# Kernel optimization log

Measured on AMD Instinct MI355X. Metric: run time of the kernel, lower is better.

The kernel has to match this reference:

```python
import jax, jax.numpy as jnp
import numpy as np

N = 20000; P = 3; L_LP = 10; L_NS = 20; D = 128; OUT = 2; E = 640000; V_LP = 5000; V_NS = 10000


def _gru(x, lengths, W_ih, W_hh, b_ih, b_hh):
    # x: [B, T, Din]; returns last valid hidden state per sequence (pack_padded semantics)
    T = x.shape[1]
    xp = jnp.einsum('btd,gd->btg', x, W_ih) + b_ih  # [B, T, 3H]
    h0 = jnp.zeros((x.shape[0], W_hh.shape[1]), x.dtype)

    def step(h, inp):
        xpt, t = inp
        hp = h @ W_hh.T + b_hh
        xr, xz, xn = jnp.split(xpt, 3, axis=-1)
        hr, hz, hn = jnp.split(hp, 3, axis=-1)
        r = jax.nn.sigmoid(xr + hr)
        z = jax.nn.sigmoid(xz + hz)
        nn_ = jnp.tanh(xn + r * hn)
        h_new = (1.0 - z) * nn_ + z * h
        h = jnp.where((t < lengths)[:, None], h_new, h)
        return h, None

    hT, _ = jax.lax.scan(step, h0, (jnp.swapaxes(xp, 0, 1), jnp.arange(T)))
    return hT


def _gcn(x, src, dst, w, W, b, n):
    # PyG GCNConv: add self-loops (weight 1), symmetric normalization by in-degree
    loops = jnp.arange(n)
    s = jnp.concatenate([src, loops])
    d = jnp.concatenate([dst, loops])
    ww = jnp.concatenate([w, jnp.ones((n,), w.dtype)])
    deg = jax.ops.segment_sum(ww, d, num_segments=n)
    dinv = jnp.where(deg > 0, 1.0 / jnp.sqrt(deg), 0.0)
    norm = dinv[s] * ww * dinv[d]
    xw = x @ W.T
    return jax.ops.segment_sum(norm[:, None] * xw[s], d, num_segments=n) + b


def _lnorm(x, g, b):
    m = jnp.mean(x, axis=-1, keepdims=True)
    v = jnp.var(x, axis=-1, keepdims=True)
    return (x - m) / jnp.sqrt(v + 1e-5) * g + b


def _forward(x_ref, x_def, x_pdt, edge_weight, lp_emb, ns_emb, lp_Wih, lp_Whh, lp_bih, lp_bhh, ns_Wih, ns_Whh, ns_bih, ns_bhh, lp_fc_W, lp_fc_b, all_fc_W, all_fc_b, conv1_W, conv1_b, conv2_W, conv2_b, conv3_W, conv3_b, ln1_g, ln1_b, ln2_g, ln2_b, mp1_W, mp1_b, mp2_W, mp2_b, idx_lp, x_lp_length, idx_ns, x_ns_length, edge_index):
    n = idx_ns.shape[0]
    # long-path GRU encodings, one GRU run per path slot (vmapped over P)
    xl = lp_emb[idx_lp]  # [N, P, L_LP, D]
    gru_lp = lambda seq, lens: _gru(seq, lens, lp_Wih, lp_Whh, lp_bih, lp_bhh)
    h_lp = jax.vmap(gru_lp, in_axes=(1, 1))(xl, x_lp_length)  # [P, N, D]
    # torch.cat(h_list).view(N, D*P): row-major reshape of [P, N, D]
    x_lp = h_lp.reshape(n, P * D) @ lp_fc_W.T + lp_fc_b
    # natural-sequence GRU encoding
    x_ns = _gru(ns_emb[idx_ns], x_ns_length, ns_Wih, ns_Whh, ns_bih, ns_bhh)  # [N, D]
    # torch.cat(dim=0).view(N, 5D): faithful row-major reshape of [5N, D]
    x = jnp.concatenate([x_pdt, x_ref, x_def, x_lp, x_ns], axis=0).reshape(n, 5 * D)
    x = x @ all_fc_W.T + all_fc_b
    src, dst = edge_index[0], edge_index[1]
    convs = [(conv1_W, conv1_b), (conv2_W, conv2_b), (conv3_W, conv3_b)]
    lns = [(ln1_g, ln1_b), (ln2_g, ln2_b)]
    emb = x
    for i in range(3):
        x = _gcn(x, src, dst, edge_weight, convs[i][0], convs[i][1], n)
        emb = x
        x = jax.nn.relu(x)
        # dropout p=0.25 omitted (eval mode)
        if i < 2:
            x = _lnorm(x, lns[i][0], lns[i][1])
    x = x @ mp1_W.T + mp1_b
    x = x @ mp2_W.T + mp2_b
    return emb, jax.nn.log_softmax(x, axis=1)


def setup_inputs() -> dict:
    ks = jax.random.split(jax.random.key(0), 40)
    f32 = jnp.float32
    nrm = lambda k, sh, s: jax.random.normal(k, sh, f32) * s
    inp = {}
    inp['idx_lp'] = jax.random.randint(ks[0], (N, P, L_LP), 0, V_LP)
    inp['x_lp_length'] = jax.random.randint(ks[1], (N, P), 1, L_LP + 1)
    inp['idx_ns'] = jax.random.randint(ks[2], (N, L_NS), 0, V_NS)
    inp['x_ns_length'] = jax.random.randint(ks[3], (N,), 1, L_NS + 1)
    inp['x_ref'] = nrm(ks[4], (N, D), 1.0)
    inp['x_def'] = nrm(ks[5], (N, D), 1.0)
    inp['x_pdt'] = nrm(ks[6], (N, D), 1.0)
    inp['edge_index'] = jax.random.randint(ks[7], (2, E), 0, N)
    inp['edge_weight'] = jax.random.uniform(ks[8], (E,), f32)
    inp['lp_emb'] = nrm(ks[9], (V_LP, D), 0.5)
    inp['ns_emb'] = nrm(ks[10], (V_NS, D), 0.5)
    s = 0.08
    inp['lp_Wih'] = nrm(ks[11], (3 * D, D), s)
    inp['lp_Whh'] = nrm(ks[12], (3 * D, D), s)
    inp['lp_bih'] = nrm(ks[13], (3 * D,), s)
    inp['lp_bhh'] = nrm(ks[14], (3 * D,), s)
    inp['ns_Wih'] = nrm(ks[15], (3 * D, D), s)
    inp['ns_Whh'] = nrm(ks[16], (3 * D, D), s)
    inp['ns_bih'] = nrm(ks[17], (3 * D,), s)
    inp['ns_bhh'] = nrm(ks[18], (3 * D,), s)
    inp['lp_fc_W'] = nrm(ks[19], (D, P * D), 0.05)
    inp['lp_fc_b'] = nrm(ks[20], (D,), 0.05)
    inp['all_fc_W'] = nrm(ks[21], (D, 5 * D), 0.05)
    inp['all_fc_b'] = nrm(ks[22], (D,), 0.05)
    inp['conv1_W'] = nrm(ks[23], (D, D), 0.08)
    inp['conv1_b'] = nrm(ks[24], (D,), 0.05)
    inp['conv2_W'] = nrm(ks[25], (D, D), 0.08)
    inp['conv2_b'] = nrm(ks[26], (D,), 0.05)
    inp['conv3_W'] = nrm(ks[27], (D, D), 0.08)
    inp['conv3_b'] = nrm(ks[28], (D,), 0.05)
    inp['ln1_g'] = jnp.ones((D,), f32)
    inp['ln1_b'] = jnp.zeros((D,), f32)
    inp['ln2_g'] = jnp.ones((D,), f32)
    inp['ln2_b'] = jnp.zeros((D,), f32)
    inp['mp1_W'] = nrm(ks[29], (D, D), 0.08)
    inp['mp1_b'] = nrm(ks[30], (D,), 0.05)
    inp['mp2_W'] = nrm(ks[31], (OUT, D), 0.08)
    inp['mp2_b'] = nrm(ks[32], (OUT,), 0.05)
    return inp


def reference(idx_lp, x_lp_length, idx_ns, x_ns_length, x_ref, x_def, x_pdt, edge_index, edge_weight, lp_emb, ns_emb, lp_Wih, lp_Whh, lp_bih, lp_bhh, ns_Wih, ns_Whh, ns_bih, ns_bhh, lp_fc_W, lp_fc_b, all_fc_W, all_fc_b, conv1_W, conv1_b, conv2_W, conv2_b, conv3_W, conv3_b, ln1_g, ln1_b, ln2_g, ln2_b, mp1_W, mp1_b, mp2_W, mp2_b):
    return _forward(x_ref, x_def, x_pdt, edge_weight, lp_emb, ns_emb, lp_Wih, lp_Whh, lp_bih, lp_bhh, ns_Wih, ns_Whh, ns_bih, ns_bhh, lp_fc_W, lp_fc_b, all_fc_W, all_fc_b, conv1_W, conv1_b, conv2_W, conv2_b, conv3_W, conv3_b, ln1_g, ln1_b, ln2_g, ln2_b, mp1_W, mp1_b, mp2_W, mp2_b, idx_lp, x_lp_length, idx_ns, x_ns_length, edge_index)
```

## Files before the change

kernel.cpp:

```cpp
#include <hip/hip_runtime.h>
#include <math.h>

typedef unsigned short u16;
typedef short bf16x4 __attribute__((ext_vector_type(4)));
typedef short bf16x8 __attribute__((ext_vector_type(8)));
typedef float f32x16 __attribute__((ext_vector_type(16)));

#define NN 20000
#define PP 3
#define TLP 10
#define TNS 20
#define DD 128
#define EE 640000

__device__ __forceinline__ float bf2f(u16 u) {
  union { unsigned u; float f; } v; v.u = ((unsigned)u) << 16; return v.f;
}
__device__ __forceinline__ u16 f2bf(float f) {
  union { float f; unsigned u; } v; v.f = f;
  unsigned r = v.u + 0x7fffu + ((v.u >> 16) & 1u);
  return (u16)(r >> 16);
}
__device__ __forceinline__ short f2bf_hw(float f) {
  __bf16 b = (__bf16)f;
  return (short)__builtin_bit_cast(unsigned short, b);
}
__device__ __forceinline__ float loadf(const void* p, size_t i, int isf) {
  return isf ? ((const float*)p)[i] : bf2f(((const u16*)p)[i]);
}
__device__ __forceinline__ float fex2(float x) { return __builtin_amdgcn_exp2f(x); }
__device__ __forceinline__ float frcp(float x) { return __builtin_amdgcn_rcpf(x); }
__device__ __forceinline__ unsigned cvtpk(float lo, float hi) {
  unsigned r; asm("v_cvt_pk_bf16_f32 %0, %1, %2" : "=v"(r) : "v"(lo), "v"(hi));
  return r;
}

__global__ void k_detect(const void* probe, int* flag, int* bins) {
  __shared__ int any;
  if (threadIdx.x == 0) any = 0;
  __syncthreads();
  if (threadIdx.x < 128) bins[threadIdx.x] = 0;
  const u16* p = (const u16*)probe;
  int bad = 0;
  for (int i = threadIdx.x; i < 4096; i += 256) {
    int e = (p[2 * i] >> 7) & 0xFF;
    if (e >= 0x9F) bad = 1;
  }
  if (bad) atomicOr(&any, 1);
  __syncthreads();
  if (threadIdx.x == 0) flag[0] = any;
}

struct CvtJobs {
  const void* src[16];
  int off[16];
  int n[16];
};

struct CvtJobsB {
  const void* src[12];
  int off[12];
  int n[12];
  int thr[12];
  float scA[12];
  float scB[12];
};

__global__ void k_cvtb(CvtJobsB j, CvtJobs jf, u16* __restrict__ dst,
                       float* __restrict__ fdst, int* __restrict__ counts,
                       const int* flag) {
  const int isf = flag[0];
  if (blockIdx.x >= 12 * 64 + 16) {
    int i = (blockIdx.x - (12 * 64 + 16)) * 256 + threadIdx.x;
    if (i < NN) counts[i] = 0;
    return;
  }
  if (blockIdx.x >= 12 * 64) {
    const int job = blockIdx.x - 12 * 64;
    const void* s = jf.src[job];
    float* d = fdst + jf.off[job];
    const int n = jf.n[job];
    for (int i = threadIdx.x; i < n; i += 256) d[i] = loadf(s, i, isf);
    return;
  }
  const int job = blockIdx.x >> 6;
  if (job < 2 && !isf) return;
  const int chunk = blockIdx.x & 63;
  const void* s = j.src[job];
  u16* d = dst + j.off[job];
  const int n = j.n[job];
  const int thr = j.thr[job];
  const float sA = j.scA[job], sB = j.scB[job];
  for (int i = chunk * 256 + threadIdx.x; i < n; i += 64 * 256)
    d[i] = f2bf(loadf(s, i, isf) * (i < thr ? sA : sB));
}

__global__ void k_lenboth(const int* __restrict__ lensLP,
                          const int* __restrict__ lensNS,
                          int* __restrict__ bins) {
  int sg = blockIdx.x * 256 + threadIdx.x;
  int lane = threadIdx.x & 63;
  int binL = 0, binN = 0;
  if (sg < PP * NN) binL = lensLP[(sg % NN) * PP + sg / NN];
  if (sg < NN) binN = lensNS[sg];
  for (int b = 1; b <= TLP; ++b) {
    unsigned long long m = __ballot(binL == b);
    if (m) {
      int leader = (int)(__ffsll((long long)m) - 1);
      if (lane == leader) atomicAdd(&bins[b], (int)__popcll(m));
    }
  }
  for (int b = 1; b <= TNS; ++b) {
    unsigned long long m = __ballot(binN == b);
    if (m) {
      int leader = (int)(__ffsll((long long)m) - 1);
      if (lane == leader) atomicAdd(&bins[64 + b], (int)__popcll(m));
    }
  }
}

__global__ void k_binscan2(int* __restrict__ bins,
                           const float* __restrict__ w_mp2,
                           const float* __restrict__ b_mp1_,
                           const float* __restrict__ b_mp2_,
                           const void* __restrict__ mp1raw,
                           float* __restrict__ Wc, const int* flag) {
  if (blockIdx.x == 0) {
    if (threadIdx.x == 0) {
      int acc = 0;
      for (int k = 0; k < 32; ++k) { bins[32 + k] = acc; acc += bins[k]; }
    }
    if (threadIdx.x == 1) {
      int acc = 0;
      for (int k = 0; k < 32; ++k) { bins[96 + k] = acc; acc += bins[64 + k]; }
    }
    return;
  }
  const int isf = flag[0];
  const int t = threadIdx.x;
  const int o = t >> 7, k = t & 127;
  float acc = 0.f;
  for (int d2 = 0; d2 < 128; ++d2)
    acc += w_mp2[o * 128 + d2] * loadf(mp1raw, (size_t)d2 * 128 + k, isf);
  Wc[t] = acc;
  if (t < 2) {
    float bacc = b_mp2_[t];
    for (int d2 = 0; d2 < 128; ++d2) bacc += w_mp2[t * 128 + d2] * b_mp1_[d2];
    Wc[256 + t] = bacc;
  }
}

__global__ void k_lenfillboth(const int* __restrict__ lensLP,
                              const int* __restrict__ lensNS,
                              int* __restrict__ bins,
                              int* __restrict__ permLP,
                              int* __restrict__ permNS) {
  int sg = blockIdx.x * 256 + threadIdx.x;
  int lane = threadIdx.x & 63;
  int binL = 0, binN = 0;
  if (sg < PP * NN) binL = lensLP[(sg % NN) * PP + sg / NN];
  if (sg < NN) binN = lensNS[sg];
  for (int b = 1; b <= TLP; ++b) {
    unsigned long long m = __ballot(binL == b);
    if (m) {
      int leader = (int)(__ffsll((long long)m) - 1);
      int base = 0;
      if (lane == leader) base = atomicAdd(&bins[32 + b], (int)__popcll(m));
      base = __shfl(base, leader);
      if (binL == b) {
        int rank = (int)__popcll(m & ((1ull << lane) - 1ull));
        permLP[base + rank] = sg;
      }
    }
  }
  for (int b = 1; b <= TNS; ++b) {
    unsigned long long m = __ballot(binN == b);
    if (m) {
      int leader = (int)(__ffsll((long long)m) - 1);
      int base = 0;
      if (lane == leader) base = atomicAdd(&bins[96 + b], (int)__popcll(m));
      base = __shfl(base, leader);
      if (binN == b) {
        int rank = (int)__popcll(m & ((1ull << lane) - 1ull));
        permNS[base + rank] = sg;
      }
    }
  }
}

__global__ __launch_bounds__(512, 2) void k_gru5(
    const int* __restrict__ permLP, const int* __restrict__ permNS, int nbNS,
    const u16* __restrict__ embLPc, const u16* __restrict__ embNSc,
    const u16* __restrict__ embLPr, const u16* __restrict__ embNSr,
    const int* __restrict__ idxLP, const int* __restrict__ idxNS,
    const int* __restrict__ lenLP, const int* __restrict__ lenNS,
    const u16* __restrict__ WihLP, const u16* __restrict__ WhhLP,
    const u16* __restrict__ WihNS, const u16* __restrict__ WhhNS,
    const float* __restrict__ bihLP, const float* __restrict__ bhhLP,
    const float* __restrict__ bihNS, const float* __restrict__ bhhNS,
    u16* __restrict__ HoutLP, u16* __restrict__ HoutNS, int nbLP,
    const int* __restrict__ e_dst, int* __restrict__ counts,
    const int* __restrict__ flag) {
  __shared__ u16 xp[2][3][128][36];
  __shared__ u16 Hbf2[2][32][132];
  __shared__ int ivs[TNS][32];
  __shared__ int rowv[32], outv[32], lenv_s[32];
  __shared__ int Tbs;

  const int bid = blockIdx.x;
  const int nGru = nbLP + nbNS;
  const int tid = threadIdx.x;
  if (bid >= nGru) {
    int e = (bid - nGru) * 512 + tid;
    if (e < EE) atomicAdd(&counts[e_dst[e]], 1);
    return;
  }
  const int isf = flag[0];
  const int isNS = bid < nbNS;
  const int chunk = isNS ? (nbNS - 1 - bid) : (nbLP - 1 - (bid - nbNS));
  const int* perm = isNS ? (permNS + chunk * 32) : (permLP + chunk * 32);
  const u16* embbf = isNS ? (isf ? embNSc : embNSr) : (isf ? embLPc : embLPr);
  const int* idx = isNS ? idxNS : idxLP;
  const int* lens = isNS ? lenNS : lenLP;
  const u16* Wih = isNS ? WihNS : WihLP;
  const u16* Whh = isNS ? WhhNS : WhhLP;
  const float* bih = isNS ? bihNS : bihLP;
  const float* bhh = isNS ? bhhNS : bhhLP;
  u16* Hout = isNS ? HoutNS : HoutLP;
  const int T = isNS ? TNS : TLP;

  const int w = tid >> 6, lane = tid & 63;
  const int l31 = lane & 31, lh = lane >> 5;
  const int role = w >> 2;
  const int j = w & 3;
  const int d = 32 * j + l31;

  if (tid < 32) {
    int sg = perm[tid];
    int row = isNS ? sg : ((sg % NN) * PP + sg / NN);
    rowv[tid] = row;
    outv[tid] = sg;
    lenv_s[tid] = lens[row];
  }
  __syncthreads();
  if (tid == 0) {
    int m = 1;
    for (int k = 0; k < 32; ++k) m = max(m, lenv_s[k]);
    Tbs = m;
  }
  __syncthreads();
  const int Tb = Tbs;

  for (int z = tid; z < Tb * 32; z += 512) {
    int s = z & 31, t = z >> 5;
    ivs[t][s] = idx[(size_t)rowv[s] * T + t];
  }
  for (int z = tid; z < 2112; z += 512) ((unsigned*)Hbf2[0])[z] = 0u;

  bf16x8 wf[24];
  {
    const u16* Ws = role ? Whh : Wih;
#pragma unroll
    for (int g = 0; g < 3; ++g)
#pragma unroll
      for (int kb = 0; kb < 8; ++kb)
        wf[g * 8 + kb] =
            *(const bf16x8*)(Ws + (size_t)(128 * g + d) * 128 + kb * 16 + lh * 8);
  }
  const float SA = -1.44269504088896f;
  const float SN = -2.88539008177793f;
  float ib0, ib1, ib2;
  if (!role) {
    ib0 = SA * (bih[d] + bhh[d]);
    ib1 = SA * (bih[128 + d] + bhh[128 + d]);
    ib2 = SN * bih[256 + d];
  } else {
    ib0 = 0.f;
    ib1 = 0.f;
    ib2 = SN * bhh[256 + d];
  }

  __syncthreads();
  int lenr[16];
#pragma unroll
  for (int rg = 0; rg < 16; ++rg)
    lenr[rg] = lenv_s[(rg & 3) + 8 * (rg >> 2) + 4 * lh];

  float h[16];
#pragma unroll
  for (int rg = 0; rg < 16; ++rg) h[rg] = 0.f;

  for (int i = 0; i <= Tb; ++i) {
    if (!role) {
      if (i < Tb) {
        bf16x8 Xf[8];
        const u16* erow = embbf + (size_t)ivs[i][l31] * 128 + lh * 8;
#pragma unroll
        for (int kb = 0; kb < 8; ++kb) Xf[kb] = *(const bf16x8*)(erow + kb * 16);
        f32x16 a0 = (f32x16)(ib0), a1 = (f32x16)(ib1), a2 = (f32x16)(ib2);
#pragma unroll
        for (int kb = 0; kb < 8; ++kb) {
          a0 = __builtin_amdgcn_mfma_f32_32x32x16_bf16(Xf[kb], wf[kb], a0, 0, 0, 0);
          a1 = __builtin_amdgcn_mfma_f32_32x32x16_bf16(Xf[kb], wf[8 + kb], a1, 0, 0, 0);
          a2 = __builtin_amdgcn_mfma_f32_32x32x16_bf16(Xf[kb], wf[16 + kb], a2, 0, 0, 0);
        }
        const int sl = i & 1;
#pragma unroll
        for (int rq = 0; rq < 4; ++rq) {
          int mo = 8 * rq + 4 * lh;
          bf16x4 p0, p1, p2;
#pragma unroll
          for (int q = 0; q < 4; ++q) {
            p0[q] = f2bf_hw(a0[4 * rq + q]);
            p1[q] = f2bf_hw(a1[4 * rq + q]);
            p2[q] = f2bf_hw(a2[4 * rq + q]);
          }
          *(bf16x4*)(&xp[sl][0][d][mo]) = p0;
          *(bf16x4*)(&xp[sl][1][d][mo]) = p1;
          *(bf16x4*)(&xp[sl][2][d][mo]) = p2;
        }
      }
    } else {
      if (i >= 1) {
        const int rs = (i - 1) & 1, wsl = i & 1;
        bf16x8 Hf[8];
#pragma unroll
        for (int kb = 0; kb < 8; ++kb) {
          bf16x4 lo = *(const bf16x4*)(&Hbf2[rs][l31][16 * kb + 8 * lh]);
          bf16x4 hi = *(const bf16x4*)(&Hbf2[rs][l31][16 * kb + 8 * lh + 4]);
          Hf[kb] = __builtin_shufflevector(lo, hi, 0, 1, 2, 3, 4, 5, 6, 7);
        }
        f32x16 a0 = (f32x16)(ib0), a1 = (f32x16)(ib1), a2 = (f32x16)(ib2);
#pragma unroll
        for (int kb = 0; kb < 8; ++kb) {
          a0 = __builtin_amdgcn_mfma_f32_32x32x16_bf16(Hf[kb], wf[kb], a0, 0, 0, 0);
          a1 = __builtin_amdgcn_mfma_f32_32x32x16_bf16(Hf[kb], wf[8 + kb], a1, 0, 0, 0);
          a2 = __builtin_amdgcn_mfma_f32_32x32x16_bf16(Hf[kb], wf[16 + kb], a2, 0, 0, 0);
        }
        const int t = i - 1;
#pragma unroll
        for (int rq = 0; rq < 4; ++rq) {
          int mo = 8 * rq + 4 * lh;
          bf16x4 x0 = *(const bf16x4*)(&xp[rs][0][d][mo]);
          bf16x4 x1 = *(const bf16x4*)(&xp[rs][1][d][mo]);
          bf16x4 x2 = *(const bf16x4*)(&xp[rs][2][d][mo]);
          float hq[4];
#pragma unroll
          for (int q = 0; q < 4; ++q) {
            int rg = 4 * rq + q;
            float r = frcp(1.f + fex2(a0[rg] + bf2f((u16)x0[q])));
            float z = frcp(1.f + fex2(a1[rg] + bf2f((u16)x1[q])));
            float s = fmaf(r, a2[rg], bf2f((u16)x2[q]));
            float nn_ = fmaf(2.f, frcp(1.f + fex2(s)), -1.f);
            float hnew = fmaf(z, h[rg] - nn_, nn_);
            h[rg] = (t < lenr[rg]) ? hnew : h[rg];
            hq[q] = h[rg];
          }
          unsigned pa = cvtpk(hq[0], hq[1]);
          unsigned pb = cvtpk(hq[2], hq[3]);
          Hbf2[wsl][mo + 0][d] = (u16)pa;
          Hbf2[wsl][mo + 1][d] = (u16)(pa >> 16);
          Hbf2[wsl][mo + 2][d] = (u16)pb;
          Hbf2[wsl][mo + 3][d] = (u16)(pb >> 16);
        }
      }
    }
    __syncthreads();
  }

  if (role) {
#pragma unroll
    for (int rg = 0; rg < 16; ++rg) {
      int m = (rg & 3) + 8 * (rg >> 2) + 4 * lh;
      Hout[(size_t)outv[m] * 128 + d] = f2bf(h[rg]);
    }
  }
}

__global__ __launch_bounds__(128) void k_gemm_mfma(
    const void* __restrict__ A0, const void* __restrict__ A1,
    const void* __restrict__ A2, const u16* __restrict__ A3,
    const u16* __restrict__ A4, int mode, int K,
    const u16* __restrict__ W, const float* __restrict__ bias,
    void* __restrict__ Cout, int out_bf, int M, const int* __restrict__ flag,
    const int* __restrict__ esrc, const int* __restrict__ edst,
    const void* __restrict__ ew, int* __restrict__ cursor,
    int2* __restrict__ csr, const int* __restrict__ startT,
    float* __restrict__ dinvOut, int tailN, int tailMode, int gemmBlocks) {
  const int isf = flag[0];
  const int tid = threadIdx.x;
  if ((int)blockIdx.x >= gemmBlocks) {
    int i = ((int)blockIdx.x - gemmBlocks) * 128 + tid;
    if (i < tailN) {
      if (tailMode == 1) {
        int s = esrc[i];
        float wv = loadf(ew, i, isf);
        int p = atomicAdd(&cursor[edst[i]], 1);
        csr[p] = make_int2(s, __float_as_int(wv));
      } else {
        int a = startT[i], b = startT[i + 1];
        float sum = 1.f;
        for (int k = a; k < b; ++k) sum += __int_as_float(csr[k].y);
        dinvOut[i] = 1.f / sqrtf(sum);
      }
    }
    return;
  }
  const int w = tid >> 6, lane = tid & 63;
  const int l31 = lane & 31, lh = lane >> 5;
  const int w23 = w;
  const int mbase = blockIdx.x * 32;
  const int row = mbase + l31;
  const int rowc = row < M ? row : M - 1;

  f32x16 acc0 = (f32x16)(0.f), acc1 = (f32x16)(0.f);
  const int nk = K >> 4;
  for (int kb = 0; kb < nk; ++kb) {
    bf16x8 a;
    if (mode == 0) {
      a = *(const bf16x8*)((const u16*)A0 + (size_t)rowc * K + kb * 16 + lh * 8);
    } else {
      int r5 = 5 * rowc + (kb >> 3);
      int slot = r5 / NN;
      int inner = r5 - slot * NN;
      int koff = (kb & 7) * 16 + lh * 8;
      if (slot < 3) {
        const void* p = (slot == 0) ? A0 : (slot == 1) ? A1 : A2;
        if (isf) {
          const float* fp = (const float*)p + (size_t)inner * 128 + koff;
          float4 v0 = *(const float4*)fp;
          float4 v1 = *(const float4*)(fp + 4);
          a[0] = (short)f2bf(v0.x); a[1] = (short)f2bf(v0.y);
          a[2] = (short)f2bf(v0.z); a[3] = (short)f2bf(v0.w);
          a[4] = (short)f2bf(v1.x); a[5] = (short)f2bf(v1.y);
          a[6] = (short)f2bf(v1.z); a[7] = (short)f2bf(v1.w);
        } else {
          a = *(const bf16x8*)((const u16*)p + (size_t)inner * 128 + koff);
        }
      } else {
        const u16* p = (slot == 3) ? A3 : A4;
        a = *(const bf16x8*)(p + (size_t)inner * 128 + koff);
      }
    }
    const u16* wp = W + (size_t)(64 * w23 + l31) * K + kb * 16 + lh * 8;
    bf16x8 b0 = *(const bf16x8*)wp;
    bf16x8 b1 = *(const bf16x8*)(wp + (size_t)32 * K);
    acc0 = __builtin_amdgcn_mfma_f32_32x32x16_bf16(a, b0, acc0, 0, 0, 0);
    acc1 = __builtin_amdgcn_mfma_f32_32x32x16_bf16(a, b1, acc1, 0, 0, 0);
  }
  const int col0 = 64 * w23 + l31;
  const float bv0 = bias ? bias[col0] : 0.f;
  const float bv1 = bias ? bias[col0 + 32] : 0.f;
#pragma unroll
  for (int rg = 0; rg < 16; ++rg) {
    int m = (rg & 3) + 8 * (rg >> 2) + 4 * lh;
    int grow = mbase + m;
    if (grow < M) {
      float v0 = acc0[rg] + bv0, v1 = acc1[rg] + bv1;
      if (out_bf) {
        ((u16*)Cout)[(size_t)grow * 128 + col0] = f2bf(v0);
        ((u16*)Cout)[(size_t)grow * 128 + col0 + 32] = f2bf(v1);
      } else {
        ((float*)Cout)[(size_t)grow * 128 + col0] = v0;
        ((float*)Cout)[(size_t)grow * 128 + col0 + 32] = v1;
      }
    }
  }
}

__global__ void k_scan(const int* __restrict__ counts, int* __restrict__ start,
                       int* __restrict__ cursor, int n) {
  __shared__ int part[256];
  const int C = (n + 255) / 256;
  int tid = threadIdx.x;
  int base = tid * C;
  int s = 0;
  for (int k = 0; k < C; ++k) {
    int i = base + k;
    s += (i < n) ? counts[i] : 0;
  }
  part[tid] = s;
  __syncthreads();
  if (tid == 0) {
    int acc = 0;
    for (int k = 0; k < 256; ++k) { int v = part[k]; part[k] = acc; acc += v; }
  }
  __syncthreads();
  int run = part[tid];
  for (int k = 0; k < C; ++k) {
    int i = base + k;
    if (i < n) {
      int c = counts[i];
      start[i] = run;
      cursor[i] = run;
      run += c;
    }
  }
  if (tid == 255) start[n] = run;
}

__global__ __launch_bounds__(256) void k_gcn_gather(
    const int* __restrict__ start, const int2* __restrict__ csr,
    const float* __restrict__ dinv, const u16* __restrict__ xwbf,
    const float* __restrict__ bias, const float* __restrict__ g,
    const float* __restrict__ b, u16* __restrict__ out_bf,
    void* __restrict__ dout, const float* __restrict__ Wc,
    const int* __restrict__ flag, int mode) {
  int v = blockIdx.x * 4 + (threadIdx.x >> 6);
  int lane = threadIdx.x & 63;
  if (v >= NN) return;
  const int c0 = 2 * lane;
  float acc0 = 0.f, acc1 = 0.f;
  int i = start[v];
  const int i1 = start[v + 1];
  for (; i + 4 <= i1; i += 4) {
    int2 e0 = csr[i], e1 = csr[i + 1], e2 = csr[i + 2], e3 = csr[i + 3];
    unsigned p0 = *(const unsigned*)(xwbf + (size_t)e0.x * 128 + c0);
    unsigned p1 = *(const unsigned*)(xwbf + (size_t)e1.x * 128 + c0);
    unsigned p2 = *(const unsigned*)(xwbf + (size_t)e2.x * 128 + c0);
    unsigned p3 = *(const unsigned*)(xwbf + (size_t)e3.x * 128 + c0);
    float f0 = __int_as_float(e0.y) * dinv[e0.x];
    float f1 = __int_as_float(e1.y) * dinv[e1.x];
    float f2 = __int_as_float(e2.y) * dinv[e2.x];
    float f3 = __int_as_float(e3.y) * dinv[e3.x];
    acc0 += f0 * bf2f((u16)(p0 & 0xffff)) + f1 * bf2f((u16)(p1 & 0xffff)) +
            f2 * bf2f((u16)(p2 & 0xffff)) + f3 * bf2f((u16)(p3 & 0xffff));
    acc1 += f0 * bf2f((u16)(p0 >> 16)) + f1 * bf2f((u16)(p1 >> 16)) +
            f2 * bf2f((u16)(p2 >> 16)) + f3 * bf2f((u16)(p3 >> 16));
  }
  if (i + 2 <= i1) {
    int2 e0 = csr[i], e1 = csr[i + 1];
    unsigned p0 = *(const unsigned*)(xwbf + (size_t)e0.x * 128 + c0);
    unsigned p1 = *(const unsigned*)(xwbf + (size_t)e1.x * 128 + c0);
    float f0 = __int_as_float(e0.y) * dinv[e0.x];
    float f1 = __int_as_float(e1.y) * dinv[e1.x];
    acc0 += f0 * bf2f((u16)(p0 & 0xffff)) + f1 * bf2f((u16)(p1 & 0xffff));
    acc1 += f0 * bf2f((u16)(p0 >> 16)) + f1 * bf2f((u16)(p1 >> 16));
    i += 2;
  }
  if (i < i1) {
    int2 e = csr[i];
    float c = __int_as_float(e.y) * dinv[e.x];
    unsigned pv = *(const unsigned*)(xwbf + (size_t)e.x * 128 + c0);
    acc0 += c * bf2f((u16)(pv & 0xffff));
    acc1 += c * bf2f((u16)(pv >> 16));
  }
  float dv = dinv[v];
  unsigned sv = *(const unsigned*)(xwbf + (size_t)v * 128 + c0);
  float y0 = bias[c0] + dv * (dv * bf2f((u16)(sv & 0xffff)) + acc0);
  float y1 = bias[c0 + 1] + dv * (dv * bf2f((u16)(sv >> 16)) + acc1);
  if (mode == 1) {
    if (flag[0]) {
      *(float2*)((float*)dout + (size_t)v * 128 + c0) = make_float2(y0, y1);
    } else {
      unsigned pk = (unsigned)f2bf(y0) | ((unsigned)f2bf(y1) << 16);
      *(unsigned*)((u16*)dout + (size_t)v * 128 + c0) = pk;
    }
    float x0 = fmaxf(y0, 0.f), x1 = fmaxf(y1, 0.f);
    float p0 = x0 * Wc[c0] + x1 * Wc[c0 + 1];
    float p1 = x0 * Wc[128 + c0] + x1 * Wc[128 + c0 + 1];
#pragma unroll
    for (int off = 32; off; off >>= 1) {
      p0 += __shfl_xor(p0, off);
      p1 += __shfl_xor(p1, off);
    }
    if (lane == 0) {
      float v0 = p0 + Wc[256], v1 = p1 + Wc[257];
      float m = fmaxf(v0, v1);
      float ls = m + logf(__expf(v0 - m) + __expf(v1 - m));
      size_t base = (size_t)NN * 128 + (size_t)v * 2;
      if (flag[0]) {
        ((float*)dout)[base + 0] = v0 - ls;
        ((float*)dout)[base + 1] = v1 - ls;
      } else {
        unsigned pk = (unsigned)f2bf(v0 - ls) | ((unsigned)f2bf(v1 - ls) << 16);
        *(unsigned*)((u16*)dout + base) = pk;
      }
    }
  } else {
    float x0 = fmaxf(y0, 0.f), x1 = fmaxf(y1, 0.f);
    float s_ = x0 + x1;
#pragma unroll
    for (int off = 32; off; off >>= 1) s_ += __shfl_xor(s_, off);
    float mean = s_ * (1.f / 128.f);
    float e0 = x0 - mean, e1 = x1 - mean;
    float vv = e0 * e0 + e1 * e1;
#pragma unroll
    for (int off = 32; off; off >>= 1) vv += __shfl_xor(vv, off);
    float inv = 1.f / sqrtf(vv * (1.f / 128.f) + 1e-5f);
    unsigned pk = (unsigned)f2bf(e0 * inv * g[c0] + b[c0]) |
                  ((unsigned)f2bf(e1 * inv * g[c0 + 1] + b[c0 + 1]) << 16);
    *(unsigned*)(out_bf + (size_t)v * 128 + c0) = pk;
  }
}

extern "C" void kernel_launch(void* const* d_in, const int* in_sizes, int n_in,
                              void* d_out, int out_size, void* d_ws, size_t ws_size,
                              hipStream_t stream) {
  const int* idx_lp = (const int*)d_in[0];
  const int* len_lp = (const int*)d_in[1];
  const int* idx_ns = (const int*)d_in[2];
  const int* len_ns = (const int*)d_in[3];
  const void* x_ref = d_in[4];
  const void* x_def = d_in[5];
  const void* x_pdt = d_in[6];
  const int* eidx   = (const int*)d_in[7];
  const void* ew    = d_in[8];
  const void* lp_emb = d_in[9];
  const void* ns_emb = d_in[10];

  char* cur = (char*)d_ws;
  auto alloc = [&](size_t bytes, size_t align) -> void* {
    size_t a = ((size_t)cur + align - 1) & ~(align - 1);
    cur = (char*)(a + bytes);
    return (void*)a;
  };
  int* flag     = (int*)alloc(64, 64);
  float* smallW = (float*)alloc(3104 * 4, 16);
  float* f_Wc   = (float*)alloc(260 * 4, 16);
  float* f_dinv = (float*)alloc(NN * 4, 16);
  int* counts   = (int*)alloc(NN * 4, 16);
  int* startA   = (int*)alloc((NN + 1) * 4, 16);
  int* cursorE  = (int*)alloc(NN * 4, 16);
  int* bins     = (int*)alloc(128 * 4, 16);
  int* perm_lp  = (int*)alloc(PP * NN * 4, 16);
  int* perm_ns  = (int*)alloc(NN * 4, 16);
  int2* csr2    = (int2*)alloc((size_t)EE * 8, 16);
  u16* ub       = (u16*)alloc((size_t)20233216 * 2, 16);
  u16* embbf_lp = ub;
  u16* embbf_ns = ub + 640000;
  u16* wg_lpih  = ub + 1920000;
  u16* wg_lphh  = ub + 1969152;
  u16* wg_nsih  = ub + 2018304;
  u16* wg_nshh  = ub + 2067456;
  u16* wg_lpfc  = ub + 2116608;
  u16* wg_allfc = ub + 2165760;
  u16* wg_c1    = ub + 2247680;
  u16* wg_c2    = ub + 2264064;
  u16* wg_c3    = ub + 2280448;
  u16* hbf_lp   = ub + 2313216;
  u16* hbf_ns   = ub + 9993216;
  u16* lp_bf    = ub + 12553216;
  u16* xcur_bf  = ub + 15113216;
  u16* xw_bf    = ub + 17673216;

  static const int fn[16] = {384, 384, 384, 384, 128, 128, 128, 128,
                             128, 128, 128, 128, 128, 128, 256, 2};
  static const int fsrc[16] = {13, 14, 17, 18, 20, 22, 24, 26,
                               28, 29, 30, 31, 32, 34, 35, 36};
  CvtJobs jf;
  int foff[16];
  {
    int off = 0;
    for (int j = 0; j < 16; ++j) {
      jf.src[j] = d_in[fsrc[j]];
      jf.off[j] = off;
      jf.n[j] = fn[j];
      foff[j] = off;
      off += fn[j];
    }
  }
  float* b_lpbih = smallW + foff[0];
  float* b_lpbhh = smallW + foff[1];
  float* b_nsbih = smallW + foff[2];
  float* b_nsbhh = smallW + foff[3];
  float* b_lpfc  = smallW + foff[4];
  float* b_allfc = smallW + foff[5];
  float* b_conv[3] = {smallW + foff[6], smallW + foff[7], smallW + foff[8]};
  float* g_ln[2] = {smallW + foff[9], smallW + foff[11]};
  float* b_ln[2] = {smallW + foff[10], smallW + foff[12]};
  float* b_mp1   = smallW + foff[13];
  float* w_mp2   = smallW + foff[14];
  float* b_mp2   = smallW + foff[15];

  static const int bn[12] = {640000, 1280000, 49152, 49152, 49152, 49152,
                             49152, 81920, 16384, 16384, 16384, 0};
  static const int bsrc[12] = {9, 10, 11, 12, 15, 16, 19, 21, 23, 25, 27, 33};
  static const int boff[12] = {0, 640000, 1920000, 1969152, 2018304, 2067456,
                               2116608, 2165760, 2247680, 2264064, 2280448,
                               2296832};
  CvtJobsB jb;
  for (int j = 0; j < 12; ++j) {
    jb.src[j] = d_in[bsrc[j]];
    jb.off[j] = boff[j];
    jb.n[j] = bn[j];
    const bool gw = (j >= 2 && j <= 5);
    jb.thr[j] = gw ? 32768 : 0;
    jb.scA[j] = gw ? -1.44269504088896f : 1.f;
    jb.scB[j] = gw ? -2.88539008177793f : 1.f;
  }

  const int* e_src = eidx;
  const int* e_dst = eidx + EE;

  k_detect<<<1, 256, 0, stream>>>(lp_emb, flag, bins);

  const int initBlocks = (NN + 255) / 256;
  k_cvtb<<<12 * 64 + 16 + initBlocks, 256, 0, stream>>>(jb, jf, ub, smallW,
                                                        counts, flag);

  k_lenboth<<<(PP * NN + 255) / 256, 256, 0, stream>>>(len_lp, len_ns, bins);
  k_binscan2<<<2, 256, 0, stream>>>(bins, w_mp2, b_mp1, b_mp2, d_in[33],
                                    f_Wc, flag);
  k_lenfillboth<<<(PP * NN + 255) / 256, 256, 0, stream>>>(len_lp, len_ns, bins,
                                                           perm_lp, perm_ns);

  const int nbLP = PP * NN / 32, nbNS = NN / 32;
  const int histBlocks = (EE + 511) / 512;
  k_gru5<<<nbLP + nbNS + histBlocks, 512, 0, stream>>>(
      perm_lp, perm_ns, nbNS, embbf_lp, embbf_ns,
      (const u16*)lp_emb, (const u16*)ns_emb,
      idx_lp, idx_ns, len_lp, len_ns,
      wg_lpih, wg_lphh, wg_nsih, wg_nshh, b_lpbih, b_lpbhh, b_nsbih, b_nsbhh,
      hbf_lp, hbf_ns, nbLP, e_dst, counts, flag);

  k_scan<<<1, 256, 0, stream>>>(counts, startA, cursorE, NN);

  const int gg = (NN + 31) / 32;
  const int fillBlocks = (EE + 127) / 128;
  const int degBlocks = (NN + 127) / 128;
  k_gemm_mfma<<<gg + fillBlocks, 128, 0, stream>>>(
      hbf_lp, nullptr, nullptr, nullptr, nullptr, 0, 384, wg_lpfc, b_lpfc,
      lp_bf, 1, NN, flag, e_src, e_dst, ew, cursorE, csr2, nullptr, nullptr,
      EE, 1, gg);
  k_gemm_mfma<<<gg + degBlocks, 128, 0, stream>>>(
      x_pdt, x_ref, x_def, lp_bf, hbf_ns, 1, 640, wg_allfc, b_allfc,
      xcur_bf, 1, NN, flag, nullptr, nullptr, nullptr, nullptr, csr2, startA,
      f_dinv, NN, 2, gg);

  const u16* wgc[3] = {wg_c1, wg_c2, wg_c3};
  for (int l = 0; l < 3; ++l) {
    k_gemm_mfma<<<gg, 128, 0, stream>>>(
        xcur_bf, nullptr, nullptr, nullptr, nullptr, 0, DD, wgc[l], nullptr,
        xw_bf, 1, NN, flag, nullptr, nullptr, nullptr, nullptr, nullptr,
        nullptr, nullptr, 0, 0, gg);
    if (l < 2) {
      k_gcn_gather<<<NN / 4, 256, 0, stream>>>(startA, csr2, f_dinv, xw_bf,
                                               b_conv[l], g_ln[l], b_ln[l],
                                               xcur_bf, nullptr, nullptr,
                                               flag, 0);
    } else {
      k_gcn_gather<<<NN / 4, 256, 0, stream>>>(startA, csr2, f_dinv, xw_bf,
                                               b_conv[l], nullptr, nullptr,
                                               nullptr, d_out, f_Wc,
                                               flag, 1);
    }
  }
}
```

Measured before the change: 898.9 us.

## Move edge histogram into length-binning kernel and fold scan into GRU launch

The per-destination edge count histogram now runs as extra blocks of the earlier k_lenboth kernel instead of as tail blocks of the GRU kernel. The exclusive scan over counts, which produces the CSR start and cursor arrays, becomes block 0 of the GRU kernel, so the separate single-block k_scan launch goes away. This cuts one kernel launch and hides the serial single-block scan behind the GRU work. In exchange, the atomic histogram now adds to the length-binning kernel's runtime, and the scan block reuses the ivs shared buffer as scratch.

```diff
diff --git a/kernel.cpp b/kernel.cpp
--- a/kernel.cpp
+++ b/kernel.cpp
@@ -97,7 +97,15 @@
 
 __global__ void k_lenboth(const int* __restrict__ lensLP,
                           const int* __restrict__ lensNS,
-                          int* __restrict__ bins) {
+                          int* __restrict__ bins,
+                          const int* __restrict__ e_dst,
+                          int* __restrict__ counts) {
+  const int nLen = (PP * NN + 255) / 256;
+  if ((int)blockIdx.x >= nLen) {
+    int e = ((int)blockIdx.x - nLen) * 256 + threadIdx.x;
+    if (e < EE) atomicAdd(&counts[e_dst[e]], 1);
+    return;
+  }
   int sg = blockIdx.x * 256 + threadIdx.x;
   int lane = threadIdx.x & 63;
   int binL = 0, binN = 0;
@@ -199,22 +207,50 @@
     const float* __restrict__ bihLP, const float* __restrict__ bhhLP,
     const float* __restrict__ bihNS, const float* __restrict__ bhhNS,
     u16* __restrict__ HoutLP, u16* __restrict__ HoutNS, int nbLP,
-    const int* __restrict__ e_dst, int* __restrict__ counts,
-    const int* __restrict__ flag) {
+    const int* __restrict__ counts, int* __restrict__ startA,
+    int* __restrict__ cursorE, const int* __restrict__ flag) {
   __shared__ u16 xp[2][3][128][36];
   __shared__ u16 Hbf2[2][32][132];
   __shared__ int ivs[TNS][32];
   __shared__ int rowv[32], outv[32], lenv_s[32];
   __shared__ int Tbs;
 
-  const int bid = blockIdx.x;
-  const int nGru = nbLP + nbNS;
   const int tid = threadIdx.x;
-  if (bid >= nGru) {
-    int e = (bid - nGru) * 512 + tid;
-    if (e < EE) atomicAdd(&counts[e_dst[e]], 1);
+  if (blockIdx.x == 0) {
+    int* part = (int*)ivs;
+    const int C = (NN + 255) / 256;
+    if (tid < 256) {
+      int base = tid * C;
+      int s = 0;
+      for (int k = 0; k < C; ++k) {
+        int i2 = base + k;
+        s += (i2 < NN) ? counts[i2] : 0;
+      }
+      part[tid] = s;
+    }
+    __syncthreads();
+    if (tid == 0) {
+      int acc = 0;
+      for (int k = 0; k < 256; ++k) { int v = part[k]; part[k] = acc; acc += v; }
+    }
+    __syncthreads();
+    if (tid < 256) {
+      int run = part[tid];
+      int base = tid * C;
+      for (int k = 0; k < C; ++k) {
+        int i2 = base + k;
+        if (i2 < NN) {
+          int c = counts[i2];
+          startA[i2] = run;
+          cursorE[i2] = run;
+          run += c;
+        }
+      }
+      if (tid == 255) startA[NN] = run;
+    }
     return;
   }
+  const int bid = blockIdx.x - 1;
   const int isf = flag[0];
   const int isNS = bid < nbNS;
   const int chunk = isNS ? (nbNS - 1 - bid) : (nbLP - 1 - (bid - nbNS));
@@ -466,37 +502,6 @@
       }
     }
   }
-}
-
-__global__ void k_scan(const int* __restrict__ counts, int* __restrict__ start,
-                       int* __restrict__ cursor, int n) {
-  __shared__ int part[256];
-  const int C = (n + 255) / 256;
-  int tid = threadIdx.x;
-  int base = tid * C;
-  int s = 0;
-  for (int k = 0; k < C; ++k) {
-    int i = base + k;
-    s += (i < n) ? counts[i] : 0;
-  }
-  part[tid] = s;
-  __syncthreads();
-  if (tid == 0) {
-    int acc = 0;
-    for (int k = 0; k < 256; ++k) { int v = part[k]; part[k] = acc; acc += v; }
-  }
-  __syncthreads();
-  int run = part[tid];
-  for (int k = 0; k < C; ++k) {
-    int i = base + k;
-    if (i < n) {
-      int c = counts[i];
-      start[i] = run;
-      cursor[i] = run;
-      run += c;
-    }
-  }
-  if (tid == 255) start[n] = run;
 }
 
 __global__ __launch_bounds__(256) void k_gcn_gather(
@@ -699,22 +704,22 @@
   k_cvtb<<<12 * 64 + 16 + initBlocks, 256, 0, stream>>>(jb, jf, ub, smallW,
                                                         counts, flag);
 
-  k_lenboth<<<(PP * NN + 255) / 256, 256, 0, stream>>>(len_lp, len_ns, bins);
+  const int lenBlocks = (PP * NN + 255) / 256;
+  const int histBlocks = (EE + 255) / 256;
+  k_lenboth<<<lenBlocks + histBlocks, 256, 0, stream>>>(len_lp, len_ns, bins,
+                                                        e_dst, counts);
   k_binscan2<<<2, 256, 0, stream>>>(bins, w_mp2, b_mp1, b_mp2, d_in[33],
                                     f_Wc, flag);
-  k_lenfillboth<<<(PP * NN + 255) / 256, 256, 0, stream>>>(len_lp, len_ns, bins,
-                                                           perm_lp, perm_ns);
+  k_lenfillboth<<<lenBlocks, 256, 0, stream>>>(len_lp, len_ns, bins,
+                                               perm_lp, perm_ns);
 
   const int nbLP = PP * NN / 32, nbNS = NN / 32;
-  const int histBlocks = (EE + 511) / 512;
-  k_gru5<<<nbLP + nbNS + histBlocks, 512, 0, stream>>>(
+  k_gru5<<<1 + nbLP + nbNS, 512, 0, stream>>>(
       perm_lp, perm_ns, nbNS, embbf_lp, embbf_ns,
       (const u16*)lp_emb, (const u16*)ns_emb,
       idx_lp, idx_ns, len_lp, len_ns,
       wg_lpih, wg_lphh, wg_nsih, wg_nshh, b_lpbih, b_lpbhh, b_nsbih, b_nsbhh,
-      hbf_lp, hbf_ns, nbLP, e_dst, counts, flag);
-
-  k_scan<<<1, 256, 0, stream>>>(counts, startA, cursorE, NN);
+      hbf_lp, hbf_ns, nbLP, counts, startA, cursorE, flag);
 
   const int gg = (NN + 31) / 32;
   const int fillBlocks = (EE + 127) / 128;
```

Result: faster. 845.2 us (-6.0%).
